# Optimization experiments

Measured on AMD Instinct MI355X. Metric: run time of the kernel, lower is better.

Reference implementation:

```python
import jax, jax.numpy as jnp
import numpy as np

PLANE_SIZE = 512
FEATURE_DIM = 8
N_LEVELS = 8
MULTISCALE = [1, 2, 4]
LOG2_PS = 9.0  # log2(plane_size)
N_SAMPLES = 1 << 20


def _build_pyramid(tex):
    # tex: [3, R, R, C] -> (flat [3, T, C], sizes [L], offsets [L]) via 2x2 box-filter mips
    levels = [tex]
    t = tex
    for _ in range(N_LEVELS - 1):
        P, h, w, C = t.shape
        t = t.reshape(P, h // 2, 2, w // 2, 2, C).mean(axis=(2, 4))
        levels.append(t)
    sizes = np.array([l.shape[1] for l in levels], dtype=np.int32)
    offsets = np.array([0] + list(np.cumsum(sizes.astype(np.int64) ** 2)[:-1]), dtype=np.int32)
    flat = jnp.concatenate([l.reshape(l.shape[0], -1, l.shape[-1]) for l in levels], axis=1)
    return flat, jnp.asarray(sizes), jnp.asarray(offsets)


def _bilinear_at_level(flat, sizes, offsets, uv, lvl_idx):
    # flat: [3, T, C]; uv: [3, N, 2] in [0,1]; lvl_idx: [3, N] int32
    szi = sizes[lvl_idx]                      # [3, N]
    sz = szi.astype(uv.dtype)
    px = uv[..., 0] * sz - 0.5                # texel centers at (i+0.5)/sz
    py = uv[..., 1] * sz - 0.5
    x0 = jnp.floor(px)
    y0 = jnp.floor(py)
    fx = (px - x0)[..., None]
    fy = (py - y0)[..., None]
    x0i = jnp.clip(x0.astype(jnp.int32), 0, szi - 1)
    x1i = jnp.clip(x0.astype(jnp.int32) + 1, 0, szi - 1)
    y0i = jnp.clip(y0.astype(jnp.int32), 0, szi - 1)
    y1i = jnp.clip(y0.astype(jnp.int32) + 1, 0, szi - 1)
    base = offsets[lvl_idx]

    def gather(yi, xi):
        idx = base + yi * szi + xi            # [3, N]
        return jax.vmap(lambda t, i: t[i])(flat, idx)  # [3, N, C]

    v00 = gather(y0i, x0i)
    v01 = gather(y0i, x1i)
    v10 = gather(y1i, x0i)
    v11 = gather(y1i, x1i)
    top = v00 * (1.0 - fx) + v01 * fx
    bot = v10 * (1.0 - fx) + v11 * fx
    return top * (1.0 - fy) + bot * fy


def _texture(grid, uv, bias):
    # mip-biased trilinear lookup (nvdiffrast linear-mipmap-linear, clamp boundary)
    flat, sizes, offsets = _build_pyramid(grid)
    max_mip = N_LEVELS - 1
    lvl = jnp.clip(bias, 0.0, float(max_mip))
    l0 = jnp.floor(lvl).astype(jnp.int32)
    l1 = jnp.minimum(l0 + 1, max_mip)
    f = (lvl - l0.astype(lvl.dtype))[..., None]
    s0 = _bilinear_at_level(flat, sizes, offsets, uv, l0)
    s1 = _bilinear_at_level(flat, sizes, offsets, uv, l1)
    return s0 * (1.0 - f) + s1 * f            # [3, N, C]


def _forward(x, level, grids):
    n = x.shape[0]
    uv = jnp.stack([x[:, [1, 2]], x[:, [0, 2]], x[:, [0, 1]]], axis=0)  # [3, N, 2]
    lvl = jnp.broadcast_to(level[:, 0][None, :], (3, n))                # [3, N]
    outs = []
    for s, g in enumerate(grids):
        enc = _texture(g, uv, lvl + LOG2_PS + float(s))                 # [3, N, C]
        outs.append(jnp.transpose(enc, (1, 0, 2)).reshape(n, 3 * FEATURE_DIM))
    return jnp.concatenate(outs, axis=-1)     # [N, 3*C*n_scales]


def setup_inputs() -> dict:
    key = jax.random.key(0)
    ks = jax.random.split(key, 5)
    x = jax.random.uniform(ks[0], (N_SAMPLES, 3), dtype=jnp.float32)
    # per-sample LOD so that bias = level + log2(plane_size) + scale spans the mip pyramid
    level = jax.random.uniform(ks[1], (N_SAMPLES, 1), dtype=jnp.float32) * (N_LEVELS - 1) - LOG2_PS
    inp = {"x": x, "level": level}
    for s, mult in enumerate(MULTISCALE):
        r = PLANE_SIZE * mult
        inp[f"grid{s}"] = jax.random.uniform(ks[2 + s], (3, r, r, FEATURE_DIM), jnp.float32, -0.01, 0.01)
    return inp


def reference(x, level, grid0, grid1, grid2):
    return _forward(x, level, (grid0, grid1, grid2))
```

## Files before the change

### kernel.cpp

```cpp
#include <hip/hip_runtime.h>

#define BLK 256
#define SBLK 576
#define NBIN 4096
#define NB 256


#define T0 0
#define T1 1048560
#define T2 2097072
#define TEX_TOTAL 3145392

__device__ __forceinline__ unsigned bfrne(float x) {
    unsigned u = __float_as_uint(x);
    return (u + 0x7fffu + ((u >> 16) & 1u)) >> 16;
}

__device__ __forceinline__ uint4 pack8(const float o[8]) {
    uint4 q;
    q.x = bfrne(o[0]) | (bfrne(o[1]) << 16);
    q.y = bfrne(o[2]) | (bfrne(o[3]) << 16);
    q.z = bfrne(o[4]) | (bfrne(o[5]) << 16);
    q.w = bfrne(o[6]) | (bfrne(o[7]) << 16);
    return q;
}

__device__ __forceinline__ void dec8(const uint4 q, float o[8]) {
    o[0] = __uint_as_float(q.x << 16);
    o[1] = __uint_as_float(q.x & 0xffff0000u);
    o[2] = __uint_as_float(q.y << 16);
    o[3] = __uint_as_float(q.y & 0xffff0000u);
    o[4] = __uint_as_float(q.z << 16);
    o[5] = __uint_as_float(q.z & 0xffff0000u);
    o[6] = __uint_as_float(q.w << 16);
    o[7] = __uint_as_float(q.w & 0xffff0000u);
}

__device__ __forceinline__ void acc8(const uint4 q, float w, float o[8]) {
    o[0] = fmaf(__uint_as_float(q.x << 16), w, o[0]);
    o[1] = fmaf(__uint_as_float(q.x & 0xffff0000u), w, o[1]);
    o[2] = fmaf(__uint_as_float(q.y << 16), w, o[2]);
    o[3] = fmaf(__uint_as_float(q.y & 0xffff0000u), w, o[3]);
    o[4] = fmaf(__uint_as_float(q.z << 16), w, o[4]);
    o[5] = fmaf(__uint_as_float(q.z & 0xffff0000u), w, o[5]);
    o[6] = fmaf(__uint_as_float(q.w << 16), w, o[6]);
    o[7] = fmaf(__uint_as_float(q.w & 0xffff0000u), w, o[7]);
}

__device__ __forceinline__ unsigned spread3(unsigned v) {
    return (v & 1u) | ((v & 2u) << 2) | ((v & 4u) << 4);
}

__device__ __forceinline__ unsigned mkey(float a, float b, float c, float lev) {
    int il = (int)(lev + 9.0f); il = min(max(il, 0), 7);
    int ia = (int)(a * 8.0f); ia = min(max(ia, 0), 7);
    int ib = (int)(b * 8.0f); ib = min(max(ib, 0), 7);
    int ic = (int)(c * 8.0f); ic = min(max(ic, 0), 7);
    unsigned m = (spread3((unsigned)ia) << 2) | (spread3((unsigned)ib) << 1) | spread3((unsigned)ic);
    return (m << 3) | (unsigned)il;
}

__global__ void __launch_bounds__(BLK) base_hist_kernel(
    const float* __restrict__ g0, const float* __restrict__ g1,
    const float* __restrict__ g2, uint4* __restrict__ wsT,
    const float* __restrict__ x, const float* __restrict__ level,
    unsigned* __restrict__ counts,
    int bA, int bB, int bC, int bBase, int n, int chunk) {
    if ((int)blockIdx.x >= bBase) {
        __shared__ unsigned h[NBIN];
        for (int b = threadIdx.x; b < NBIN; b += BLK) h[b] = 0;
        __syncthreads();
        int blk = blockIdx.x - bBase;
        int lo = blk * chunk, hi = min(lo + chunk, n);
        for (int i = lo + (int)threadIdx.x; i < hi; i += BLK) {
            unsigned key = mkey(x[3 * i], x[3 * i + 1], x[3 * i + 2], level[i]);
            atomicAdd(&h[key], 1u);
        }
        __syncthreads();
        for (int b = threadIdx.x; b < NBIN; b += BLK)
            counts[(size_t)b * NB + blk] = h[b];
        return;
    }
    int j = blockIdx.x * BLK + threadIdx.x;
    if (j >= bC) return;
    if (j < bA) {
        const float4* sp = (const float4*)g0 + (size_t)j * 2;
        float4 a = sp[0], b = sp[1];
        float o[8] = {a.x, a.y, a.z, a.w, b.x, b.y, b.z, b.w};
        wsT[T0 + j] = pack8(o);
    } else if (j < bB) {
        int t = j - bA;
        int p = t >> 18;
        int rem = t & ((1 << 18) - 1);
        int y = rem >> 9;
        int x2 = rem & 511;
        const float4* sp = (const float4*)g1 + (size_t)p * 1024 * 1024 * 2;
        float o[8] = {0, 0, 0, 0, 0, 0, 0, 0};
#pragma unroll
        for (int dy = 0; dy < 2; ++dy) {
#pragma unroll
            for (int dx = 0; dx < 2; ++dx) {
                size_t idx = ((size_t)(2 * y + dy) * 1024 + (2 * x2 + dx)) * 2;
                float4 a = sp[idx], b = sp[idx + 1];
                o[0] += a.x; o[1] += a.y; o[2] += a.z; o[3] += a.w;
                o[4] += b.x; o[5] += b.y; o[6] += b.z; o[7] += b.w;
            }
        }
#pragma unroll
        for (int c = 0; c < 8; ++c) o[c] *= 0.25f;
        wsT[T1 + t] = pack8(o);
    } else {
        int t = j - bB;
        int p = t >> 18;
        int rem = t & ((1 << 18) - 1);
        int y = rem >> 9;
        int x2 = rem & 511;
        const float4* sp = (const float4*)g2 + (size_t)p * 2048 * 2048 * 2;
        float o[8] = {0, 0, 0, 0, 0, 0, 0, 0};
#pragma unroll
        for (int dy = 0; dy < 4; ++dy) {
#pragma unroll
            for (int dx = 0; dx < 4; ++dx) {
                size_t idx = ((size_t)(4 * y + dy) * 2048 + (4 * x2 + dx)) * 2;
                float4 a = sp[idx], b = sp[idx + 1];
                o[0] += a.x; o[1] += a.y; o[2] += a.z; o[3] += a.w;
                o[4] += b.x; o[5] += b.y; o[6] += b.z; o[7] += b.w;
            }
        }
#pragma unroll
        for (int c = 0; c < 8; ++c) o[c] *= 0.0625f;
        wsT[T2 + t] = pack8(o);
    }
}

__device__ __forceinline__ void down2b_body(
    uint4* __restrict__ wsT, int j,
    int srcA, int dstA, int lszA, int bA,
    int srcB, int dstB, int lszB, int bB,
    int srcC, int dstC, int lszC, int bC) {
    if (j >= bC) return;
    int src, dst, lsz;
    if (j < bA) {
        src = srcA; dst = dstA; lsz = lszA;
    } else if (j < bB) {
        src = srcB; dst = dstB; lsz = lszB; j -= bA;
    } else {
        src = srcC; dst = dstC; lsz = lszC; j -= bB;
    }
    int sz = 1 << lsz;
    int p = j >> (2 * lsz);
    int rem = j & (sz * sz - 1);
    int y = rem >> lsz;
    int x = rem & (sz - 1);
    int S = sz << 1;
    const uint4* sp = wsT + src + (size_t)p * S * S;
    size_t i00 = (size_t)(2 * y) * S + 2 * x;
    float d0[8], d1[8], d2[8], d3[8];
    dec8(sp[i00], d0);
    dec8(sp[i00 + 1], d1);
    dec8(sp[i00 + S], d2);
    dec8(sp[i00 + S + 1], d3);
    float o[8];
#pragma unroll
    for (int c = 0; c < 8; ++c) o[c] = (d0[c] + d1[c] + d2[c] + d3[c]) * 0.25f;
    wsT[dst + (size_t)(p << (2 * lsz)) + rem] = pack8(o);
}

__global__ void __launch_bounds__(BLK) down2b_kernel(
    uint4* __restrict__ wsT,
    int srcA, int dstA, int lszA, int bA,
    int srcB, int dstB, int lszB, int bB,
    int srcC, int dstC, int lszC, int bC) {
    down2b_body(wsT, blockIdx.x * BLK + threadIdx.x,
                srcA, dstA, lszA, bA, srcB, dstB, lszB, bB, srcC, dstC, lszC, bC);
}

__global__ void __launch_bounds__(BLK) scanA_down_kernel(
    uint4* __restrict__ wsT, unsigned* __restrict__ counts,
    unsigned* __restrict__ binTotal, int nScan,
    int srcA, int dstA, int lszA, int bA,
    int srcB, int dstB, int lszB, int bB,
    int srcC, int dstC, int lszC, int bC) {
    if ((int)blockIdx.x < nScan) {
        __shared__ unsigned tmp[NB];
        int bin = blockIdx.x, t = threadIdx.x;
        unsigned v = counts[(size_t)bin * NB + t];
        tmp[t] = v;
        __syncthreads();
        for (int d = 1; d < NB; d <<= 1) {
            unsigned u = (t >= d) ? tmp[t - d] : 0u;
            __syncthreads();
            tmp[t] += u;
            __syncthreads();
        }
        counts[(size_t)bin * NB + t] = tmp[t] - v;
        if (t == NB - 1) binTotal[bin] = tmp[t];
        return;
    }
    down2b_body(wsT, (blockIdx.x - nScan) * BLK + threadIdx.x,
                srcA, dstA, lszA, bA, srcB, dstB, lszB, bB, srcC, dstC, lszC, bC);
}

__global__ void __launch_bounds__(BLK) scanB_down_kernel(
    uint4* __restrict__ wsT, const unsigned* __restrict__ binTotal,
    unsigned* __restrict__ binBase,
    int srcA, int dstA, int lszA, int bA,
    int srcB, int dstB, int lszB, int bB,
    int srcC, int dstC, int lszC, int bC) {
    if (blockIdx.x == 0) {
        __shared__ unsigned tmp[BLK];
        int t = threadIdx.x;
        unsigned v[16];
        unsigned sum = 0;
#pragma unroll
        for (int k = 0; k < 16; ++k) {
            v[k] = binTotal[t * 16 + k];
            sum += v[k];
        }
        tmp[t] = sum;
        __syncthreads();
        for (int d = 1; d < BLK; d <<= 1) {
            unsigned u = (t >= d) ? tmp[t - d] : 0u;
            __syncthreads();
            tmp[t] += u;
            __syncthreads();
        }
        unsigned run = tmp[t] - sum;
#pragma unroll
        for (int k = 0; k < 16; ++k) {
            binBase[t * 16 + k] = run;
            run += v[k];
        }
        return;
    }
    down2b_body(wsT, (blockIdx.x - 1) * BLK + threadIdx.x,
                srcA, dstA, lszA, bA, srcB, dstB, lszB, bB, srcC, dstC, lszC, bC);
}

__global__ void __launch_bounds__(BLK) scatter_down_kernel(
    uint4* __restrict__ wsT,
    const float* __restrict__ x, const float* __restrict__ level,
    const unsigned* __restrict__ prefix, const unsigned* __restrict__ binBase,
    float4* __restrict__ xs, unsigned* __restrict__ perm, int n, int chunk,
    int srcA, int dstA, int lszA, int bA,
    int srcB, int dstB, int lszB, int bB,
    int srcC, int dstC, int lszC, int bC) {
    if ((int)blockIdx.x < NB) {
        __shared__ unsigned h[NBIN];
        for (int b = threadIdx.x; b < NBIN; b += BLK) h[b] = 0;
        __syncthreads();
        int blk = blockIdx.x;
        int lo = blk * chunk, hi = min(lo + chunk, n);
        for (int i = lo + (int)threadIdx.x; i < hi; i += BLK) {
            float a = x[3 * i], b = x[3 * i + 1], c = x[3 * i + 2];
            float lv = level[i];
            unsigned key = mkey(a, b, c, lv);
            unsigned r = atomicAdd(&h[key], 1u);
            unsigned pos = binBase[key] + prefix[(size_t)key * NB + blk] + r;
            xs[pos] = make_float4(a, b, c, lv);
            perm[pos] = (unsigned)i;
        }
        return;
    }
    down2b_body(wsT, (blockIdx.x - NB) * BLK + threadIdx.x,
                srcA, dstA, lszA, bA, srcB, dstB, lszB, bB, srcC, dstC, lszC, bC);
}

__device__ __forceinline__ void addr4(const uint4* __restrict__ t, int sz,
                                      float u, float v,
                                      const uint4** a, float* w) {
    float fsz = (float)sz;
    float px = u * fsz - 0.5f;
    float py = v * fsz - 0.5f;
    float x0f = floorf(px), y0f = floorf(py);
    float fx = px - x0f, fy = py - y0f;
    int xi = (int)x0f, yi = (int)y0f;
    int m = sz - 1;
    int x0 = min(max(xi, 0), m);
    int x1 = min(max(xi + 1, 0), m);
    int y0 = min(max(yi, 0), m);
    int y1 = min(max(yi + 1, 0), m);
    const uint4* r0 = t + (size_t)y0 * sz;
    const uint4* r1 = t + (size_t)y1 * sz;
    a[0] = r0 + x0;
    a[1] = r0 + x1;
    a[2] = r1 + x0;
    a[3] = r1 + x1;
    w[0] = (1.0f - fx) * (1.0f - fy);
    w[1] = fx * (1.0f - fy);
    w[2] = (1.0f - fx) * fy;
    w[3] = fx * fy;
}

__global__ void __launch_bounds__(SBLK) tex_sample_kernel(
    const float4* __restrict__ xs, const unsigned* __restrict__ perm,
    const uint4* __restrict__ wsT, float* __restrict__ out, int n) {
    __shared__ float so[64][75];
    __shared__ unsigned soi[64];
    int nblk = gridDim.x;
    int cpx = nblk >> 3;
    int bid = blockIdx.x;
    int bswz = (bid & 7) * cpx + (bid >> 3);
    int base = bswz * 64;
    if (base >= n) return;
    int lane = threadIdx.x & 63;
    int wv = threadIdx.x >> 6;
    int s = (wv * 11) >> 5;
    int p = wv - 3 * s;
    int j = base + lane;
    bool valid = j < n;

    if (valid) {
        float4 xl = xs[j];
        if (wv == 0) soi[lane] = perm[j];

        const int WSS_[3] = {T0, T1, T2};
        const int OFFMIN_[3] = {0, 1048576, 5242880};

        const int R = 512 << s;
        float bias = xl.w + 9.0f + (float)s;
        float lvl = fminf(fmaxf(bias, 0.0f), 7.0f);
        float l0f = floorf(lvl);
        int l0 = (int)l0f;
        int l1 = min(l0 + 1, 7);
        float f = lvl - l0f;
        int sz0 = R >> l0;
        int sz1 = R >> l1;
        int off0 = ((R * R - sz0 * sz0) * 4) / 3;
        int off1 = ((R * R - sz1 * sz1) * 4) / 3;
        const uint4* base0 = wsT + WSS_[s] + (size_t)3 * (off0 - OFFMIN_[s]);
        const uint4* base1 = wsT + WSS_[s] + (size_t)3 * (off1 - OFFMIN_[s]);

        float u = (p == 0) ? xl.y : xl.x;
        float v = (p == 2) ? xl.y : xl.z;
        const uint4* ap[8];
        float w0[4], w1[4];
        addr4(base0 + (size_t)p * (sz0 * sz0), sz0, u, v, &ap[0], w0);
        addr4(base1 + (size_t)p * (sz1 * sz1), sz1, u, v, &ap[4], w1);
        uint4 q[8];
#pragma unroll
        for (int t = 0; t < 8; ++t) q[t] = *ap[t];

        float a[8] = {0, 0, 0, 0, 0, 0, 0, 0};
        float b[8] = {0, 0, 0, 0, 0, 0, 0, 0};
#pragma unroll
        for (int t = 0; t < 4; ++t) acc8(q[t], w0[t], a);
#pragma unroll
        for (int t = 0; t < 4; ++t) acc8(q[4 + t], w1[t], b);
        float omf = 1.0f - f;
        int c0 = s * 24 + p * 8;
#pragma unroll
        for (int c = 0; c < 8; ++c)
            so[lane][c0 + c] = a[c] * omf + b[c] * f;
    }
    __syncthreads();
    int nsmp = min(64, n - base);
    int lim = nsmp * 18;
#pragma unroll
    for (int k = 0; k < 2; ++k) {
        int e = k * SBLK + (int)threadIdx.x;
        if (e < lim) {
            int sample = (e * 3641) >> 16;
            int word = e - 18 * sample;
            float4 v;
            v.x = so[sample][word * 4 + 0];
            v.y = so[sample][word * 4 + 1];
            v.z = so[sample][word * 4 + 2];
            v.w = so[sample][word * 4 + 3];
            *(float4*)(out + (size_t)soi[sample] * 72 + word * 4) = v;
        }
    }
}

extern "C" void kernel_launch(void* const* d_in, const int* in_sizes, int n_in,
                              void* d_out, int out_size, void* d_ws, size_t ws_size,
                              hipStream_t stream) {
    const float* x = (const float*)d_in[0];
    const float* level = (const float*)d_in[1];
    const float* g0 = (const float*)d_in[2];
    const float* g1 = (const float*)d_in[3];
    const float* g2 = (const float*)d_in[4];
    float* out = (float*)d_out;
    uint4* wsT = (uint4*)d_ws;
    int n = in_sizes[0] / 3;

    float4* xs = (float4*)(wsT + TEX_TOTAL);
    unsigned* perm = (unsigned*)(xs + n);
    unsigned* counts = perm + n;
    unsigned* binTotal = counts + (size_t)NBIN * NB;
    unsigned* binBase = binTotal + NBIN;

    auto lvlOff = [](int s, int l) -> int {
        const int WSS[3] = {T0, T1, T2};
        const int OFFMIN[3] = {0, 1048576, 5242880};
        int R = 512 << s;
        int sz = R >> l;
        int off = ((R * R - sz * sz) * 4) / 3;
        return WSS[s] + 3 * (off - OFFMIN[s]);
    };

    int chunk = (n + NB - 1) / NB;

    {
        int bA = 3 * 512 * 512;
        int bB = bA * 2;
        int bC = bA * 3;
        int bBase = (bC + BLK - 1) / BLK;
        base_hist_kernel<<<bBase + NB, BLK, 0, stream>>>(
            g0, g1, g2, wsT, x, level, counts, bA, bB, bC, bBase, n, chunk);
    }

    auto segs = [&](int l, int& srcA, int& dstA, int& lszA, int& bA,
                    int& srcB, int& dstB, int& lszB, int& bB,
                    int& srcC, int& dstC, int& lszC, int& bC) {
        int szA = 512 >> l;
        bA = 3 * szA * szA;
        srcA = lvlOff(0, l - 1); dstA = lvlOff(0, l); lszA = 9 - l;
        bB = bA; srcB = 0; dstB = 0; lszB = 0;
        bC = bA; srcC = 0; dstC = 0; lszC = 0;
        if (l >= 2) {
            int szB = 1024 >> l;
            bB = bA + 3 * szB * szB;
            srcB = lvlOff(1, l - 1); dstB = lvlOff(1, l); lszB = 10 - l;
            bC = bB;
        }
        if (l >= 3) {
            int szC = 2048 >> l;
            bC = bB + 3 * szC * szC;
            srcC = lvlOff(2, l - 1); dstC = lvlOff(2, l); lszC = 11 - l;
        }
    };

    int srcA, dstA, lszA, bA, srcB, dstB, lszB, bB, srcC, dstC, lszC, bC;

    segs(1, srcA, dstA, lszA, bA, srcB, dstB, lszB, bB, srcC, dstC, lszC, bC);
    {
        int nDown = (bC + BLK - 1) / BLK;
        scanA_down_kernel<<<NBIN + nDown, BLK, 0, stream>>>(
            wsT, counts, binTotal, NBIN,
            srcA, dstA, lszA, bA, srcB, dstB, lszB, bB, srcC, dstC, lszC, bC);
    }
    segs(2, srcA, dstA, lszA, bA, srcB, dstB, lszB, bB, srcC, dstC, lszC, bC);
    {
        int nDown = (bC + BLK - 1) / BLK;
        scanB_down_kernel<<<1 + nDown, BLK, 0, stream>>>(
            wsT, binTotal, binBase,
            srcA, dstA, lszA, bA, srcB, dstB, lszB, bB, srcC, dstC, lszC, bC);
    }
    segs(3, srcA, dstA, lszA, bA, srcB, dstB, lszB, bB, srcC, dstC, lszC, bC);
    {
        int nDown = (bC + BLK - 1) / BLK;
        scatter_down_kernel<<<NB + nDown, BLK, 0, stream>>>(
            wsT, x, level, counts, binBase, xs, perm, n, chunk,
            srcA, dstA, lszA, bA, srcB, dstB, lszB, bB, srcC, dstC, lszC, bC);
    }
    for (int l = 4; l <= 7; ++l) {
        segs(l, srcA, dstA, lszA, bA, srcB, dstB, lszB, bB, srcC, dstC, lszC, bC);
        down2b_kernel<<<(bC + BLK - 1) / BLK, BLK, 0, stream>>>(
            wsT, srcA, dstA, lszA, bA, srcB, dstB, lszB, bB, srcC, dstC, lszC, bC);
    }

    int nblk = (n + 63) / 64;
    nblk = (nblk + 7) & ~7;
    tex_sample_kernel<<<nblk, SBLK, 0, stream>>>(xs, perm, wsT, out, n);
}
```

Measured before the change: 422.0 us.

## Fuse mip tail into one kernel; one wave per scale handles all planes

The four launches that built mip levels 4-7 one at a time become a single kernel. It computes each tail texel directly from level 3 with a k×k box average, so three launch boundaries go away at the cost of redundant reads from level 3. The sampling kernel now uses 192 threads, with each wave handling one scale and all three planes per sample instead of one plane per wave. It also skips the second-level fetches when the trilinear fraction is zero. Output stores are now done per scale in 96-byte chunks per sample rather than full 288-byte rows, which may reduce write coalescing, and register pressure rises with 24 outstanding loads.

Result: slower. 433.4 us (+2.7%).

```diff
diff --git a/kernel.cpp b/kernel.cpp
--- a/kernel.cpp
+++ b/kernel.cpp
@@ -1,7 +1,7 @@
 #include <hip/hip_runtime.h>
 
 #define BLK 256
-#define SBLK 576
+#define SBLK 192
 #define NBIN 4096
 #define NB 256
 
@@ -58,6 +58,15 @@
     int ic = (int)(c * 8.0f); ic = min(max(ic, 0), 7);
     unsigned m = (spread3((unsigned)ia) << 2) | (spread3((unsigned)ib) << 1) | spread3((unsigned)ic);
     return (m << 3) | (unsigned)il;
+}
+
+__device__ __forceinline__ int lvlOffD(int s, int l) {
+    const int WSS[3] = {T0, T1, T2};
+    const int OFFMIN[3] = {0, 1048576, 5242880};
+    int R = 512 << s;
+    int sz = R >> l;
+    int off = ((R * R - sz * sz) * 4) / 3;
+    return WSS[s] + 3 * (off - OFFMIN[s]);
 }
 
 __global__ void __launch_bounds__(BLK) base_hist_kernel(
@@ -164,15 +173,6 @@
 #pragma unroll
     for (int c = 0; c < 8; ++c) o[c] = (d0[c] + d1[c] + d2[c] + d3[c]) * 0.25f;
     wsT[dst + (size_t)(p << (2 * lsz)) + rem] = pack8(o);
-}
-
-__global__ void __launch_bounds__(BLK) down2b_kernel(
-    uint4* __restrict__ wsT,
-    int srcA, int dstA, int lszA, int bA,
-    int srcB, int dstB, int lszB, int bB,
-    int srcC, int dstC, int lszC, int bC) {
-    down2b_body(wsT, blockIdx.x * BLK + threadIdx.x,
-                srcA, dstA, lszA, bA, srcB, dstB, lszB, bB, srcC, dstC, lszC, bC);
 }
 
 __global__ void __launch_bounds__(BLK) scanA_down_kernel(
@@ -264,6 +264,44 @@
     }
     down2b_body(wsT, (blockIdx.x - NB) * BLK + threadIdx.x,
                 srcA, dstA, lszA, bA, srcB, dstB, lszB, bB, srcC, dstC, lszC, bC);
+}
+
+__global__ void __launch_bounds__(BLK) down_tail_kernel(uint4* __restrict__ wsT, int total) {
+    int j = blockIdx.x * BLK + threadIdx.x;
+    if (j >= total) return;
+    int rem = j, s = 0, l = 4;
+    for (int ss = 0; ss < 3; ++ss) {
+        bool done = false;
+        for (int ll = 4; ll <= 7; ++ll) {
+            int sz_ = (512 << ss) >> ll;
+            int cnt = 3 * sz_ * sz_;
+            if (rem < cnt) { s = ss; l = ll; done = true; break; }
+            rem -= cnt;
+        }
+        if (done) break;
+    }
+    int sz = (512 << s) >> l;
+    int p = rem / (sz * sz);
+    int t = rem - p * (sz * sz);
+    int y = t / sz;
+    int x = t - y * sz;
+    int sz3 = 64 << s;
+    const uint4* sp = wsT + lvlOffD(s, 3) + (size_t)p * sz3 * sz3;
+    int k = 1 << (l - 3);
+    float o[8] = {0, 0, 0, 0, 0, 0, 0, 0};
+    for (int dy = 0; dy < k; ++dy) {
+        const uint4* row = sp + (size_t)(y * k + dy) * sz3 + x * k;
+        for (int dx = 0; dx < k; ++dx) {
+            float d[8];
+            dec8(row[dx], d);
+#pragma unroll
+            for (int c = 0; c < 8; ++c) o[c] += d[c];
+        }
+    }
+    float inv = 1.0f / (float)(k * k);
+#pragma unroll
+    for (int c = 0; c < 8; ++c) o[c] *= inv;
+    wsT[lvlOffD(s, l) + (size_t)p * sz * sz + y * sz + x] = pack8(o);
 }
 
 __device__ __forceinline__ void addr4(const uint4* __restrict__ t, int sz,
@@ -295,7 +333,7 @@
 __global__ void __launch_bounds__(SBLK) tex_sample_kernel(
     const float4* __restrict__ xs, const unsigned* __restrict__ perm,
     const uint4* __restrict__ wsT, float* __restrict__ out, int n) {
-    __shared__ float so[64][75];
+    __shared__ float so[3][64][25];
     __shared__ unsigned soi[64];
     int nblk = gridDim.x;
     int cpx = nblk >> 3;
@@ -304,21 +342,20 @@
     int base = bswz * 64;
     if (base >= n) return;
     int lane = threadIdx.x & 63;
-    int wv = threadIdx.x >> 6;
-    int s = (wv * 11) >> 5;
-    int p = wv - 3 * s;
+    int s = threadIdx.x >> 6;
     int j = base + lane;
     bool valid = j < n;
 
     if (valid) {
         float4 xl = xs[j];
-        if (wv == 0) soi[lane] = perm[j];
+        float xv0 = xl.x, xv1 = xl.y, xv2 = xl.z, lev = xl.w;
+        if (s == 0) soi[lane] = perm[j];
 
         const int WSS_[3] = {T0, T1, T2};
         const int OFFMIN_[3] = {0, 1048576, 5242880};
 
         const int R = 512 << s;
-        float bias = xl.w + 9.0f + (float)s;
+        float bias = lev + 9.0f + (float)s;
         float lvl = fminf(fmaxf(bias, 0.0f), 7.0f);
         float l0f = floorf(lvl);
         int l0 = (int)l0f;
@@ -331,43 +368,63 @@
         const uint4* base0 = wsT + WSS_[s] + (size_t)3 * (off0 - OFFMIN_[s]);
         const uint4* base1 = wsT + WSS_[s] + (size_t)3 * (off1 - OFFMIN_[s]);
 
-        float u = (p == 0) ? xl.y : xl.x;
-        float v = (p == 2) ? xl.y : xl.z;
-        const uint4* ap[8];
-        float w0[4], w1[4];
-        addr4(base0 + (size_t)p * (sz0 * sz0), sz0, u, v, &ap[0], w0);
-        addr4(base1 + (size_t)p * (sz1 * sz1), sz1, u, v, &ap[4], w1);
-        uint4 q[8];
-#pragma unroll
-        for (int t = 0; t < 8; ++t) q[t] = *ap[t];
-
-        float a[8] = {0, 0, 0, 0, 0, 0, 0, 0};
-        float b[8] = {0, 0, 0, 0, 0, 0, 0, 0};
-#pragma unroll
-        for (int t = 0; t < 4; ++t) acc8(q[t], w0[t], a);
-#pragma unroll
-        for (int t = 0; t < 4; ++t) acc8(q[4 + t], w1[t], b);
+        const uint4* ap[24];
+        float w[6][4];
+#pragma unroll
+        for (int p = 0; p < 3; ++p) {
+            float u = (p == 0) ? xv1 : xv0;
+            float v = (p == 2) ? xv1 : xv2;
+            addr4(base0 + (size_t)p * (sz0 * sz0), sz0, u, v, &ap[8 * p], w[2 * p]);
+            addr4(base1 + (size_t)p * (sz1 * sz1), sz1, u, v, &ap[8 * p + 4], w[2 * p + 1]);
+        }
+        bool doL1 = f > 0.0f;
+        uint4 q[24];
+#pragma unroll
+        for (int p = 0; p < 3; ++p)
+#pragma unroll
+            for (int t = 0; t < 4; ++t) q[8 * p + t] = *ap[8 * p + t];
+        if (doL1) {
+#pragma unroll
+            for (int p = 0; p < 3; ++p)
+#pragma unroll
+                for (int t = 0; t < 4; ++t) q[8 * p + 4 + t] = *ap[8 * p + 4 + t];
+        }
+
         float omf = 1.0f - f;
-        int c0 = s * 24 + p * 8;
-#pragma unroll
-        for (int c = 0; c < 8; ++c)
-            so[lane][c0 + c] = a[c] * omf + b[c] * f;
+#pragma unroll
+        for (int p = 0; p < 3; ++p) {
+            float a[8] = {0, 0, 0, 0, 0, 0, 0, 0};
+#pragma unroll
+            for (int t = 0; t < 4; ++t) acc8(q[8 * p + t], w[2 * p][t], a);
+            if (doL1) {
+                float b[8] = {0, 0, 0, 0, 0, 0, 0, 0};
+#pragma unroll
+                for (int t = 0; t < 4; ++t) acc8(q[8 * p + 4 + t], w[2 * p + 1][t], b);
+#pragma unroll
+                for (int c = 0; c < 8; ++c)
+                    so[s][lane][8 * p + c] = a[c] * omf + b[c] * f;
+            } else {
+#pragma unroll
+                for (int c = 0; c < 8; ++c)
+                    so[s][lane][8 * p + c] = a[c];
+            }
+        }
     }
     __syncthreads();
-    int nsmp = min(64, n - base);
-    int lim = nsmp * 18;
-#pragma unroll
-    for (int k = 0; k < 2; ++k) {
-        int e = k * SBLK + (int)threadIdx.x;
-        if (e < lim) {
-            int sample = (e * 3641) >> 16;
-            int word = e - 18 * sample;
-            float4 v;
-            v.x = so[sample][word * 4 + 0];
-            v.y = so[sample][word * 4 + 1];
-            v.z = so[sample][word * 4 + 2];
-            v.w = so[sample][word * 4 + 3];
-            *(float4*)(out + (size_t)soi[sample] * 72 + word * 4) = v;
+    if (valid) {
+#pragma unroll
+        for (int k = 0; k < 6; ++k) {
+            int e = k * 64 + lane;
+            int sample = (e * 10923) >> 16;
+            int word = e - 6 * sample;
+            if (base + sample < n) {
+                float4 v;
+                v.x = so[s][sample][word * 4 + 0];
+                v.y = so[s][sample][word * 4 + 1];
+                v.z = so[s][sample][word * 4 + 2];
+                v.w = so[s][sample][word * 4 + 3];
+                *(float4*)(out + (size_t)soi[sample] * 72 + s * 24 + word * 4) = v;
+            }
         }
     }
 }
@@ -454,10 +511,14 @@
             wsT, x, level, counts, binBase, xs, perm, n, chunk,
             srcA, dstA, lszA, bA, srcB, dstB, lszB, bB, srcC, dstC, lszC, bC);
     }
-    for (int l = 4; l <= 7; ++l) {
-        segs(l, srcA, dstA, lszA, bA, srcB, dstB, lszB, bB, srcC, dstC, lszC, bC);
-        down2b_kernel<<<(bC + BLK - 1) / BLK, BLK, 0, stream>>>(
-            wsT, srcA, dstA, lszA, bA, srcB, dstB, lszB, bB, srcC, dstC, lszC, bC);
+    {
+        int total = 0;
+        for (int s = 0; s < 3; ++s)
+            for (int l = 4; l <= 7; ++l) {
+                int sz = (512 << s) >> l;
+                total += 3 * sz * sz;
+            }
+        down_tail_kernel<<<(total + BLK - 1) / BLK, BLK, 0, stream>>>(wsT, total);
     }
 
     int nblk = (n + 63) / 64;
```
